# Kernel tuning notes

Hardware: AMD Instinct MI355X
Metric: run time of the kernel (lower is better)

Reference implementation:

```python
import jax, jax.numpy as jnp
import numpy as np


def _fft_upsample2(x):
    """Ideal (sinc) 2x upsample via FFT zero-padding, with Nyquist-bin splitting.
    x: [B, C, H, W] real -> [B, C, 2H, 2W] real."""
    H, W = x.shape[-2], x.shape[-1]
    hh, hw = H // 2, W // 2
    # shifted spectrum: index i along length-H axis <-> frequency i - H/2
    X = jnp.fft.fftshift(jnp.fft.fft2(x), axes=(-2, -1))
    Y = jnp.zeros(x.shape[:-2] + (2 * H, 2 * W), X.dtype)
    Y = Y.at[..., hh:hh + H, hw:hw + W].set(X)
    # split Nyquist row -H/2 (index hh) into +/-H/2 (indices hh and hh+H), each half
    Y = Y.at[..., hh, :].multiply(0.5)
    Y = Y.at[..., hh + H, :].set(Y[..., hh, :])
    # same for Nyquist column
    Y = Y.at[..., :, hw].multiply(0.5)
    Y = Y.at[..., :, hw + W].set(Y[..., :, hw])
    y = jnp.fft.ifft2(jnp.fft.ifftshift(Y, axes=(-2, -1))).real
    return (y * 4.0).astype(x.dtype)  # up**2 amplitude correction


def _lpf_rect_1d(N, cutoff):
    # create_lpf_rect from alias_free_convnets: ideal rect LPF in frequency
    cl = int(N * cutoff) // 2
    ch = N - cl
    rect = np.ones(N, dtype=np.float32)
    rect[cl + 1:ch] = 0.0
    if N % 4 == 0:  # half-weight on the exact cutoff (Nyquist-of-subband) bins
        rect[cl] = 0.5
        rect[ch] = 0.5
    return rect


def _lpf_rfft(x, cutoff=0.5):
    """Ideal low-pass via rfft2 with rectangular separable mask."""
    H, W = x.shape[-2], x.shape[-1]
    rect_h = _lpf_rect_1d(H, cutoff)
    rect_w = _lpf_rect_1d(W, cutoff)
    mask = jnp.asarray(rect_h[:, None] * rect_w[None, :W // 2 + 1])
    X = jnp.fft.rfft2(x) * mask
    return jnp.fft.irfft2(X, s=(H, W)).astype(x.dtype)


def setup_inputs() -> dict:
    key = jax.random.key(0)
    x = jax.random.normal(key, (8, 256, 64, 64), dtype=jnp.float32)
    return {"x": x}


def reference(x):
    u = _fft_upsample2(x)          # [B, C, 2H, 2W]
    a = jax.nn.silu(u)
    f = _lpf_rfft(a, cutoff=0.5)   # [B, C, 2H, 2W]
    return f[:, :, ::2, ::2]       # [B, C, H, W]
```

## Files before the change

### kernel.cpp

```cpp
#include <hip/hip_runtime.h>
#include <math.h>

#define TPB 256

typedef _Float16 f16x8 __attribute__((ext_vector_type(8)));
typedef float    f32x4 __attribute__((ext_vector_type(4)));

#define MFMA16(A, B, C) __builtin_amdgcn_mfma_f32_16x16x32_f16((A), (B), (C), 0, 0, 0)


__global__ __launch_bounds__(TPB, 3) void warped_mfma(const float* __restrict__ xin,
                                                      float* __restrict__ outp) {
  constexpr int SK = 72;
  constexpr int SL = 136;
  constexpr int SZ = 65;

  __shared__ __attribute__((aligned(16))) unsigned char bufA[128 * SL * 2];
  __shared__ __attribute__((aligned(16))) unsigned char bufB[128 * SK * 2];
  __shared__ float k1d[128];

  _Float16* const W0  = (_Float16*)bufA;
  _Float16* const W2  = (_Float16*)bufA;
  float*    const Z4t = (float*)bufA;
  _Float16* const W1  = (_Float16*)bufB;
  _Float16* const W3  = (_Float16*)bufB;

  const int tid = threadIdx.x;
  const int w = tid >> 6;
  const int lane = tid & 63;
  const int lq = lane >> 4;
  const int ln = lane & 15;

  const float* __restrict__ x = xin + (size_t)blockIdx.x * 4096;
  float* __restrict__ out     = outp + (size_t)blockIdx.x * 4096;

  if (tid < 128) {
    const int d = tid;
    float s = 1.0f + ((d & 1) ? 0.0f : ((d & 2) ? -1.0f : 1.0f));
    for (int f = 1; f <= 31; ++f) {
      int r = (f * d) & 127;
      s += 2.0f * __cosf((float)r * 0.04908738521234052f );
    }
    k1d[d] = s * (1.0f / 64.0f);
  }
  __syncthreads();

#pragma unroll
  for (int rep = 0; rep < 4; ++rep) {
    int idx = tid + rep * TPB;
    float4 v = ((const float4*)x)[idx];
    int i = idx >> 4, j0 = (idx & 15) << 2;
    W0[(j0 + 0) * SK + i] = (_Float16)v.x;
    W0[(j0 + 1) * SK + i] = (_Float16)v.y;
    W0[(j0 + 2) * SK + i] = (_Float16)v.z;
    W0[(j0 + 3) * SK + i] = (_Float16)v.w;
  }

  f16x8 AK[2][2], AT[4];
#pragma unroll
  for (int mt = 0; mt < 2; ++mt)
#pragma unroll
    for (int ks = 0; ks < 2; ++ks) {
      const int m = (2 * w + mt) * 16 + ln;
      f16x8 a;
#pragma unroll
      for (int j = 0; j < 8; ++j) {
        int k = ks * 32 + lq * 8 + j;
        a[j] = (_Float16)k1d[(m - 2 * k) & 127];
      }
      AK[mt][ks] = a;
    }
#pragma unroll
  for (int ks = 0; ks < 4; ++ks) {
    const int q = 16 * w + ln;
    f16x8 a;
#pragma unroll
    for (int j = 0; j < 8; ++j) {
      int k = ks * 32 + lq * 8 + j;
      a[j] = (_Float16)k1d[(k - 2 * q) & 127];
    }
    AT[ks] = a;
  }
  __syncthreads();

  const f32x4 vzero = {0.0f, 0.0f, 0.0f, 0.0f};

  {
    f32x4 acc[2][4];
#pragma unroll
    for (int mt = 0; mt < 2; ++mt)
#pragma unroll
      for (int nt = 0; nt < 4; ++nt) acc[mt][nt] = vzero;
#pragma unroll
    for (int ks = 0; ks < 2; ++ks) {
      f16x8 B[4];
#pragma unroll
      for (int nt = 0; nt < 4; ++nt)
        B[nt] = *(const f16x8*)(W0 + (nt * 16 + ln) * SK + ks * 32 + lq * 8);
#pragma unroll
      for (int mt = 0; mt < 2; ++mt)
#pragma unroll
        for (int nt = 0; nt < 4; ++nt) acc[mt][nt] = MFMA16(AK[mt][ks], B[nt], acc[mt][nt]);
    }
    __syncthreads();
#pragma unroll
    for (int mt = 0; mt < 2; ++mt)
#pragma unroll
      for (int nt = 0; nt < 4; ++nt)
#pragma unroll
        for (int r = 0; r < 4; ++r)
          W1[((2 * w + mt) * 16 + lq * 4 + r) * SK + nt * 16 + ln] = (_Float16)acc[mt][nt][r];
  }
  __syncthreads();

  {
    f32x4 acc[2][8];
#pragma unroll
    for (int mt = 0; mt < 2; ++mt)
#pragma unroll
      for (int nt = 0; nt < 8; ++nt) acc[mt][nt] = vzero;
#pragma unroll
    for (int ks = 0; ks < 2; ++ks) {
#pragma unroll
      for (int nt = 0; nt < 8; ++nt) {
        f16x8 B = *(const f16x8*)(W1 + (nt * 16 + ln) * SK + ks * 32 + lq * 8);
        acc[0][nt] = MFMA16(AK[0][ks], B, acc[0][nt]);
        acc[1][nt] = MFMA16(AK[1][ks], B, acc[1][nt]);
      }
    }
#pragma unroll
    for (int mt = 0; mt < 2; ++mt)
#pragma unroll
      for (int nt = 0; nt < 8; ++nt)
#pragma unroll
        for (int r = 0; r < 4; ++r) {
          float u = acc[mt][nt][r];
          float s = u * __builtin_amdgcn_rcpf(1.0f + __expf(-u));
          W2[((2 * w + mt) * 16 + lq * 4 + r) * SL + nt * 16 + ln] = (_Float16)s;
        }
  }
  __syncthreads();

  {
    f32x4 acc[8];
#pragma unroll
    for (int nt = 0; nt < 8; ++nt) acc[nt] = vzero;
#pragma unroll
    for (int ks = 0; ks < 4; ++ks)
#pragma unroll
      for (int nt = 0; nt < 8; ++nt) {
        f16x8 B = *(const f16x8*)(W2 + (nt * 16 + ln) * SL + ks * 32 + lq * 8);
        acc[nt] = MFMA16(AT[ks], B, acc[nt]);
      }
    __syncthreads();
#pragma unroll
    for (int nt = 0; nt < 8; ++nt)
#pragma unroll
      for (int r = 0; r < 4; ++r)
        W3[(16 * w + lq * 4 + r) * SL + nt * 16 + ln] = (_Float16)acc[nt][r];
  }
  __syncthreads();

  {
    f32x4 acc[4];
#pragma unroll
    for (int nt = 0; nt < 4; ++nt) acc[nt] = vzero;
#pragma unroll
    for (int ks = 0; ks < 4; ++ks)
#pragma unroll
      for (int nt = 0; nt < 4; ++nt) {
        f16x8 B = *(const f16x8*)(W3 + (nt * 16 + ln) * SL + ks * 32 + lq * 8);
        acc[nt] = MFMA16(AT[ks], B, acc[nt]);
      }
    __syncthreads();
#pragma unroll
    for (int nt = 0; nt < 4; ++nt)
#pragma unroll
      for (int r = 0; r < 4; ++r)
        Z4t[(16 * w + lq * 4 + r) * SZ + nt * 16 + ln] = 0.25f * acc[nt][r];
  }
  __syncthreads();

#pragma unroll
  for (int rep = 0; rep < 4; ++rep) {
    int a = (tid >> 4) + rep * 16;
    int b0 = (tid & 15) << 2;
    float4 o;
    o.x = Z4t[(b0 + 0) * SZ + a];
    o.y = Z4t[(b0 + 1) * SZ + a];
    o.z = Z4t[(b0 + 2) * SZ + a];
    o.w = Z4t[(b0 + 3) * SZ + a];
    ((float4*)out)[(a * 64 + b0) >> 2] = o;
  }
}

extern "C" void kernel_launch(void* const* d_in, const int* in_sizes, int n_in,
                              void* d_out, int out_size, void* d_ws, size_t ws_size,
                              hipStream_t stream) {
  const float* x = (const float*)d_in[0];
  float* out = (float*)d_out;
  const int nimg = in_sizes[0] / 4096;
  warped_mfma<<<dim3(nimg), dim3(TPB), 0, stream>>>(x, out);
}
```

Measured before the change: 100.3 us.

## Process two images per block with register-resident DFT operators and packed fp16 stores

Each block now loops over two images (the grid is halved), so the per-block kernel-table setup and the operator fragments held in registers (AK, BT) are amortised across images. The GEMMs are reoriented so the constant operators sit on the other MFMA operand, which lets accumulator outputs be written with packed 4-wide fp16 stores (cvt_pkrtz) instead of scalar transposed stores. The input load is no longer transposed on entry. In exchange there are fewer blocks and less parallelism per launch, more registers are held, and extra syncs are added per loop iteration.

```diff
diff --git a/kernel.cpp b/kernel.cpp
--- a/kernel.cpp
+++ b/kernel.cpp
@@ -9,30 +9,36 @@
 #define MFMA16(A, B, C) __builtin_amdgcn_mfma_f32_16x16x32_f16((A), (B), (C), 0, 0, 0)
 
 
+__device__ __forceinline__ void store4h(_Float16* p, float a0, float a1, float a2, float a3) {
+  float2 q;
+  q.x = __builtin_bit_cast(float, __builtin_amdgcn_cvt_pkrtz(a0, a1));
+  q.y = __builtin_bit_cast(float, __builtin_amdgcn_cvt_pkrtz(a2, a3));
+  *(float2*)p = q;
+}
+
 __global__ __launch_bounds__(TPB, 3) void warped_mfma(const float* __restrict__ xin,
-                                                      float* __restrict__ outp) {
-  constexpr int SK = 72;
-  constexpr int SL = 136;
-  constexpr int SZ = 65;
-
-  __shared__ __attribute__((aligned(16))) unsigned char bufA[128 * SL * 2];
-  __shared__ __attribute__((aligned(16))) unsigned char bufB[128 * SK * 2];
+                                                      float* __restrict__ outp, int nimg) {
+  constexpr int SA = 72;
+  constexpr int SB = 136;
+  constexpr int SZ = 68;
+
+  __shared__ __attribute__((aligned(16))) unsigned char bufA[128 * SB * 2];
+  __shared__ __attribute__((aligned(16))) unsigned char bufB[128 * SA * 2];
   __shared__ float k1d[128];
 
-  _Float16* const W0  = (_Float16*)bufA;
-  _Float16* const W2  = (_Float16*)bufA;
-  float*    const Z4t = (float*)bufA;
-  _Float16* const W1  = (_Float16*)bufB;
-  _Float16* const W3  = (_Float16*)bufB;
+  _Float16* const buf0 = (_Float16*)bufA;
+  _Float16* const buf2 = (_Float16*)bufA;
+  float*    const buf4 = (float*)bufA;
+  _Float16* const buf1 = (_Float16*)bufB;
+  _Float16* const buf3 = (_Float16*)bufB;
 
   const int tid = threadIdx.x;
-  const int w = tid >> 6;
   const int lane = tid & 63;
+  const int w  = tid >> 6;
+  const int wk = w >> 1;
+  const int wd = w & 1;
   const int lq = lane >> 4;
   const int ln = lane & 15;
-
-  const float* __restrict__ x = xin + (size_t)blockIdx.x * 4096;
-  float* __restrict__ out     = outp + (size_t)blockIdx.x * 4096;
 
   if (tid < 128) {
     const int d = tid;
@@ -45,152 +51,186 @@
   }
   __syncthreads();
 
-#pragma unroll
-  for (int rep = 0; rep < 4; ++rep) {
-    int idx = tid + rep * TPB;
-    float4 v = ((const float4*)x)[idx];
-    int i = idx >> 4, j0 = (idx & 15) << 2;
-    W0[(j0 + 0) * SK + i] = (_Float16)v.x;
-    W0[(j0 + 1) * SK + i] = (_Float16)v.y;
-    W0[(j0 + 2) * SK + i] = (_Float16)v.z;
-    W0[(j0 + 3) * SK + i] = (_Float16)v.w;
-  }
-
-  f16x8 AK[2][2], AT[4];
-#pragma unroll
-  for (int mt = 0; mt < 2; ++mt)
+  f16x8 AK[4][2];
+#pragma unroll
+  for (int t = 0; t < 4; ++t)
 #pragma unroll
     for (int ks = 0; ks < 2; ++ks) {
-      const int m = (2 * w + mt) * 16 + ln;
-      f16x8 a;
+      const int a = (wk * 4 + t) * 16 + ln;
+      f16x8 f;
 #pragma unroll
       for (int j = 0; j < 8; ++j) {
         int k = ks * 32 + lq * 8 + j;
-        a[j] = (_Float16)k1d[(m - 2 * k) & 127];
-      }
-      AK[mt][ks] = a;
-    }
-#pragma unroll
-  for (int ks = 0; ks < 4; ++ks) {
-    const int q = 16 * w + ln;
-    f16x8 a;
-#pragma unroll
-    for (int j = 0; j < 8; ++j) {
-      int k = ks * 32 + lq * 8 + j;
-      a[j] = (_Float16)k1d[(k - 2 * q) & 127];
-    }
-    AT[ks] = a;
-  }
-  __syncthreads();
+        f[j] = (_Float16)k1d[(a - 2 * k) & 127];
+      }
+      AK[t][ks] = f;
+    }
+  f16x8 BT[2][4];
+#pragma unroll
+  for (int t = 0; t < 2; ++t)
+#pragma unroll
+    for (int ks = 0; ks < 4; ++ks) {
+      const int c = (wk * 2 + t) * 16 + ln;
+      f16x8 f;
+#pragma unroll
+      for (int j = 0; j < 8; ++j) {
+        int k = ks * 32 + lq * 8 + j;
+        f[j] = (_Float16)k1d[(k - 2 * c) & 127];
+      }
+      BT[t][ks] = f;
+    }
 
   const f32x4 vzero = {0.0f, 0.0f, 0.0f, 0.0f};
 
-  {
-    f32x4 acc[2][4];
-#pragma unroll
-    for (int mt = 0; mt < 2; ++mt)
-#pragma unroll
-      for (int nt = 0; nt < 4; ++nt) acc[mt][nt] = vzero;
-#pragma unroll
-    for (int ks = 0; ks < 2; ++ks) {
-      f16x8 B[4];
-#pragma unroll
-      for (int nt = 0; nt < 4; ++nt)
-        B[nt] = *(const f16x8*)(W0 + (nt * 16 + ln) * SK + ks * 32 + lq * 8);
-#pragma unroll
-      for (int mt = 0; mt < 2; ++mt)
-#pragma unroll
-        for (int nt = 0; nt < 4; ++nt) acc[mt][nt] = MFMA16(AK[mt][ks], B[nt], acc[mt][nt]);
-    }
-    __syncthreads();
-#pragma unroll
-    for (int mt = 0; mt < 2; ++mt)
-#pragma unroll
-      for (int nt = 0; nt < 4; ++nt)
-#pragma unroll
-        for (int r = 0; r < 4; ++r)
-          W1[((2 * w + mt) * 16 + lq * 4 + r) * SK + nt * 16 + ln] = (_Float16)acc[mt][nt][r];
-  }
-  __syncthreads();
-
-  {
-    f32x4 acc[2][8];
-#pragma unroll
-    for (int mt = 0; mt < 2; ++mt)
-#pragma unroll
-      for (int nt = 0; nt < 8; ++nt) acc[mt][nt] = vzero;
-#pragma unroll
-    for (int ks = 0; ks < 2; ++ks) {
-#pragma unroll
-      for (int nt = 0; nt < 8; ++nt) {
-        f16x8 B = *(const f16x8*)(W1 + (nt * 16 + ln) * SK + ks * 32 + lq * 8);
-        acc[0][nt] = MFMA16(AK[0][ks], B, acc[0][nt]);
-        acc[1][nt] = MFMA16(AK[1][ks], B, acc[1][nt]);
-      }
-    }
-#pragma unroll
-    for (int mt = 0; mt < 2; ++mt)
-#pragma unroll
-      for (int nt = 0; nt < 8; ++nt)
-#pragma unroll
-        for (int r = 0; r < 4; ++r) {
-          float u = acc[mt][nt][r];
-          float s = u * __builtin_amdgcn_rcpf(1.0f + __expf(-u));
-          W2[((2 * w + mt) * 16 + lq * 4 + r) * SL + nt * 16 + ln] = (_Float16)s;
-        }
-  }
-  __syncthreads();
-
-  {
-    f32x4 acc[8];
-#pragma unroll
-    for (int nt = 0; nt < 8; ++nt) acc[nt] = vzero;
-#pragma unroll
-    for (int ks = 0; ks < 4; ++ks)
-#pragma unroll
-      for (int nt = 0; nt < 8; ++nt) {
-        f16x8 B = *(const f16x8*)(W2 + (nt * 16 + ln) * SL + ks * 32 + lq * 8);
-        acc[nt] = MFMA16(AT[ks], B, acc[nt]);
-      }
-    __syncthreads();
-#pragma unroll
-    for (int nt = 0; nt < 8; ++nt)
-#pragma unroll
-      for (int r = 0; r < 4; ++r)
-        W3[(16 * w + lq * 4 + r) * SL + nt * 16 + ln] = (_Float16)acc[nt][r];
-  }
-  __syncthreads();
-
-  {
-    f32x4 acc[4];
-#pragma unroll
-    for (int nt = 0; nt < 4; ++nt) acc[nt] = vzero;
-#pragma unroll
-    for (int ks = 0; ks < 4; ++ks)
-#pragma unroll
-      for (int nt = 0; nt < 4; ++nt) {
-        f16x8 B = *(const f16x8*)(W3 + (nt * 16 + ln) * SL + ks * 32 + lq * 8);
-        acc[nt] = MFMA16(AT[ks], B, acc[nt]);
-      }
-    __syncthreads();
-#pragma unroll
-    for (int nt = 0; nt < 4; ++nt)
-#pragma unroll
-      for (int r = 0; r < 4; ++r)
-        Z4t[(16 * w + lq * 4 + r) * SZ + nt * 16 + ln] = 0.25f * acc[nt][r];
-  }
-  __syncthreads();
-
-#pragma unroll
-  for (int rep = 0; rep < 4; ++rep) {
-    int a = (tid >> 4) + rep * 16;
-    int b0 = (tid & 15) << 2;
-    float4 o;
-    o.x = Z4t[(b0 + 0) * SZ + a];
-    o.y = Z4t[(b0 + 1) * SZ + a];
-    o.z = Z4t[(b0 + 2) * SZ + a];
-    o.w = Z4t[(b0 + 3) * SZ + a];
-    ((float4*)out)[(a * 64 + b0) >> 2] = o;
+  for (int img = blockIdx.x; img < nimg; img += gridDim.x) {
+    const float* __restrict__ x = xin + (size_t)img * 4096;
+    float* __restrict__ out     = outp + (size_t)img * 4096;
+
+#pragma unroll
+    for (int rep = 0; rep < 4; ++rep) {
+      int idx = rep * 256 + tid;
+      float4 v = ((const float4*)x)[idx];
+      int i = idx >> 4, j0 = (idx & 15) << 2;
+      store4h(buf0 + i * SA + j0, v.x, v.y, v.z, v.w);
+    }
+    __syncthreads();
+
+    {
+      f32x4 acc[2][4];
+#pragma unroll
+      for (int mtl = 0; mtl < 2; ++mtl)
+#pragma unroll
+        for (int ntl = 0; ntl < 4; ++ntl) acc[mtl][ntl] = vzero;
+#pragma unroll
+      for (int ks = 0; ks < 2; ++ks) {
+        f16x8 Ad[2];
+#pragma unroll
+        for (int mtl = 0; mtl < 2; ++mtl)
+          Ad[mtl] = *(const f16x8*)(buf0 + ((wd * 2 + mtl) * 16 + ln) * SA + ks * 32 + lq * 8);
+#pragma unroll
+        for (int mtl = 0; mtl < 2; ++mtl)
+#pragma unroll
+          for (int ntl = 0; ntl < 4; ++ntl)
+            acc[mtl][ntl] = MFMA16(Ad[mtl], AK[ntl][ks], acc[mtl][ntl]);
+      }
+#pragma unroll
+      for (int mtl = 0; mtl < 2; ++mtl)
+#pragma unroll
+        for (int ntl = 0; ntl < 4; ++ntl) {
+          int n0 = (wk * 4 + ntl) * 16, m0 = (wd * 2 + mtl) * 16;
+          f32x4 a = acc[mtl][ntl];
+          store4h(buf1 + (n0 + ln) * SA + m0 + lq * 4, a[0], a[1], a[2], a[3]);
+        }
+    }
+    __syncthreads();
+
+#pragma unroll
+    for (int nh = 0; nh < 2; ++nh) {
+      f32x4 acc[4][2];
+#pragma unroll
+      for (int mtl = 0; mtl < 4; ++mtl)
+#pragma unroll
+        for (int ntl = 0; ntl < 2; ++ntl) acc[mtl][ntl] = vzero;
+#pragma unroll
+      for (int ks = 0; ks < 2; ++ks) {
+        f16x8 Bd[2];
+#pragma unroll
+        for (int ntl = 0; ntl < 2; ++ntl)
+          Bd[ntl] =
+              *(const f16x8*)(buf1 + ((wd * 4 + nh * 2 + ntl) * 16 + ln) * SA + ks * 32 + lq * 8);
+#pragma unroll
+        for (int mtl = 0; mtl < 4; ++mtl)
+#pragma unroll
+          for (int ntl = 0; ntl < 2; ++ntl)
+            acc[mtl][ntl] = MFMA16(AK[mtl][ks], Bd[ntl], acc[mtl][ntl]);
+      }
+#pragma unroll
+      for (int mtl = 0; mtl < 4; ++mtl)
+#pragma unroll
+        for (int ntl = 0; ntl < 2; ++ntl) {
+          int n0 = (wd * 4 + nh * 2 + ntl) * 16, m0 = (wk * 4 + mtl) * 16;
+          float s[4];
+#pragma unroll
+          for (int r = 0; r < 4; ++r) {
+            float u = acc[mtl][ntl][r];
+            s[r] = u * __builtin_amdgcn_rcpf(1.0f + __expf(-u));
+          }
+          store4h(buf2 + (n0 + ln) * SB + m0 + lq * 4, s[0], s[1], s[2], s[3]);
+        }
+    }
+    __syncthreads();
+
+    {
+      f32x4 acc[4][2];
+#pragma unroll
+      for (int mtl = 0; mtl < 4; ++mtl)
+#pragma unroll
+        for (int ntl = 0; ntl < 2; ++ntl) acc[mtl][ntl] = vzero;
+#pragma unroll
+      for (int ks = 0; ks < 4; ++ks) {
+        f16x8 Ad[4];
+#pragma unroll
+        for (int mtl = 0; mtl < 4; ++mtl)
+          Ad[mtl] = *(const f16x8*)(buf2 + ((wd * 4 + mtl) * 16 + ln) * SB + ks * 32 + lq * 8);
+#pragma unroll
+        for (int mtl = 0; mtl < 4; ++mtl)
+#pragma unroll
+          for (int ntl = 0; ntl < 2; ++ntl)
+            acc[mtl][ntl] = MFMA16(Ad[mtl], BT[ntl][ks], acc[mtl][ntl]);
+      }
+#pragma unroll
+      for (int mtl = 0; mtl < 4; ++mtl)
+#pragma unroll
+        for (int ntl = 0; ntl < 2; ++ntl) {
+          int n0 = (wk * 2 + ntl) * 16, m0 = (wd * 4 + mtl) * 16;
+          f32x4 a = acc[mtl][ntl];
+          store4h(buf3 + (n0 + ln) * SB + m0 + lq * 4, a[0], a[1], a[2], a[3]);
+        }
+    }
+    __syncthreads();
+
+    {
+      f32x4 acc[2][2];
+#pragma unroll
+      for (int mtl = 0; mtl < 2; ++mtl)
+#pragma unroll
+        for (int ntl = 0; ntl < 2; ++ntl) acc[mtl][ntl] = vzero;
+#pragma unroll
+      for (int ks = 0; ks < 4; ++ks) {
+        f16x8 Ad[2];
+#pragma unroll
+        for (int mtl = 0; mtl < 2; ++mtl)
+          Ad[mtl] = *(const f16x8*)(buf3 + ((wd * 2 + mtl) * 16 + ln) * SB + ks * 32 + lq * 8);
+#pragma unroll
+        for (int mtl = 0; mtl < 2; ++mtl)
+#pragma unroll
+          for (int ntl = 0; ntl < 2; ++ntl)
+            acc[mtl][ntl] = MFMA16(Ad[mtl], BT[ntl][ks], acc[mtl][ntl]);
+      }
+#pragma unroll
+      for (int mtl = 0; mtl < 2; ++mtl)
+#pragma unroll
+        for (int ntl = 0; ntl < 2; ++ntl) {
+          int n0 = (wk * 2 + ntl) * 16, m0 = (wd * 2 + mtl) * 16;
+          f32x4 o = acc[mtl][ntl];
+          o[0] *= 0.25f; o[1] *= 0.25f; o[2] *= 0.25f; o[3] *= 0.25f;
+          *(f32x4*)(buf4 + (n0 + ln) * SZ + m0 + lq * 4) = o;
+        }
+    }
+    __syncthreads();
+
+#pragma unroll
+    for (int rep = 0; rep < 4; ++rep) {
+      int a = (tid >> 4) + rep * 16;
+      int b0 = (tid & 15) << 2;
+      float4 o;
+      o.x = buf4[(b0 + 0) * SZ + a];
+      o.y = buf4[(b0 + 1) * SZ + a];
+      o.z = buf4[(b0 + 2) * SZ + a];
+      o.w = buf4[(b0 + 3) * SZ + a];
+      ((float4*)out)[(a * 64 + b0) >> 2] = o;
+    }
+    __syncthreads();
   }
 }
 
@@ -200,5 +240,6 @@
   const float* x = (const float*)d_in[0];
   float* out = (float*)d_out;
   const int nimg = in_sizes[0] / 4096;
-  warped_mfma<<<dim3(nimg), dim3(TPB), 0, stream>>>(x, out);
+  const int grid = (nimg + 1) / 2;
+  warped_mfma<<<dim3(grid), dim3(TPB), 0, stream>>>(x, out, nimg);
 }
```

Result: faster. 96.54 us (-3.8%).
